# Kernel optimization log

Hardware: AMD Instinct MI355X
Metric: run time of the kernel (lower is better)

Reference implementation:

```python
import jax, jax.numpy as jnp
import numpy as np
from jax import lax
from functools import lru_cache

WS = 8       # window size
SS = 4       # shift size
NH = 8       # attention heads
D_STATE = 64
D_CONV = 4
CHUNK = 256  # SSD chunk length


def _ln(x, w, b, eps=1e-5):
    mu = x.mean(-1, keepdims=True)
    xc = x - mu
    var = (xc * xc).mean(-1, keepdims=True)
    return xc * lax.rsqrt(var + eps) * w + b


@lru_cache(maxsize=None)
def _rel_index(ws):
    coords = np.stack(np.meshgrid(np.arange(ws), np.arange(ws), indexing='ij')).reshape(2, -1)
    rel = (coords[:, :, None] - coords[:, None, :]).transpose(1, 2, 0)
    rel[:, :, 0] += ws - 1
    rel[:, :, 1] += ws - 1
    rel[:, :, 0] *= 2 * ws - 1
    return jnp.asarray(rel.sum(-1))  # (N, N)


@lru_cache(maxsize=None)
def _shift_mask(H, W, ws, ss):
    img = np.zeros((H, W))
    cnt = 0
    for hs in (slice(0, -ws), slice(-ws, -ss), slice(-ss, None)):
        for wsl in (slice(0, -ws), slice(-ws, -ss), slice(-ss, None)):
            img[hs, wsl] = cnt
            cnt += 1
    mw = img.reshape(H // ws, ws, W // ws, ws).transpose(0, 2, 1, 3).reshape(-1, ws * ws)
    diff = mw[:, None, :] - mw[:, :, None]
    return jnp.asarray(np.where(diff != 0, -100.0, 0.0).astype(np.float32))  # (nW,N,N)


def _segsum(a):
    # a: (...,Q) -> (...,Q,Q) with S[i,j] = sum_{k=j+1..i} a_k for i>=j else -inf
    T = a.shape[-1]
    cs = jnp.cumsum(a, -1)
    d = cs[..., :, None] - cs[..., None, :]
    return jnp.where(jnp.tril(jnp.ones((T, T), bool)), d, -jnp.inf)


def _ssd(xd, a, Bc, Cc):
    # Chunked SSD scan (Mamba2). xd=(B,L,H,P) pre-multiplied by dt; a=dt*A (B,L,H);
    # Bc,Cc=(B,L,N) with ngroups=1 (shared across heads).
    B_, L, H_, P = xd.shape
    Q = CHUNK
    c = L // Q
    N = Bc.shape[-1]
    xd = xd.reshape(B_, c, Q, H_, P)
    a = a.reshape(B_, c, Q, H_).transpose(0, 3, 1, 2)  # (B,H,c,Q)
    Bc = Bc.reshape(B_, c, Q, N)
    Cc = Cc.reshape(B_, c, Q, N)
    A_cs = jnp.cumsum(a, -1)
    Lm = jnp.exp(_segsum(a))  # (B,H,c,Q,Q) causal decay mask
    Yd = jnp.einsum('bcln,bcsn,bhcls,bcshp->bclhp', Cc, Bc, Lm, xd)
    dec_st = jnp.exp(A_cs[..., -1:] - A_cs)
    states = jnp.einsum('bcsn,bhcs,bcshp->bchpn', Bc, dec_st, xd)  # (B,c,H,P,N)
    chunk_dec = jnp.exp(A_cs[..., -1])  # (B,H,c)

    def step(h, inp):
        dec, st = inp
        return h * dec[..., None, None] + st, h

    h0 = jnp.zeros((B_, H_, P, N), xd.dtype)
    _, st_in = lax.scan(step, h0, (chunk_dec.transpose(2, 0, 1), states.transpose(1, 0, 2, 3, 4)))
    st_in = st_in.transpose(1, 0, 2, 3, 4)  # (B,c,H,P,N) state entering each chunk
    Yo = jnp.einsum('bcln,bchpn,bhcl->bclhp', Cc, st_in, jnp.exp(A_cs))
    return (Yd + Yo).reshape(B_, L, H_, P)


def _mamba2(x, win, conv_w, conv_b, dt_bias, a_log, d_skip, norm_w, wout):
    Bb, L, _ = x.shape
    conv_dim = conv_w.shape[0]
    d_inner = conv_dim - 2 * D_STATE
    nh = a_log.shape[0]
    hd = d_inner // nh
    zxbcdt = x @ win
    z = zxbcdt[..., :d_inner]
    xBC = zxbcdt[..., d_inner:d_inner + conv_dim]
    dt = zxbcdt[..., -nh:]
    # causal depthwise conv (kernel D_CONV) + SiLU
    xp = jnp.pad(xBC, ((0, 0), (D_CONV - 1, 0), (0, 0)))
    xc = conv_b + sum(xp[:, k:k + L, :] * conv_w[:, k] for k in range(D_CONV))
    xc = jax.nn.silu(xc)
    xs = xc[..., :d_inner].reshape(Bb, L, nh, hd)
    Bm = xc[..., d_inner:d_inner + D_STATE]
    Cm = xc[..., d_inner + D_STATE:]
    dt = jax.nn.softplus(dt + dt_bias)  # (B,L,nh)
    a = dt * (-jnp.exp(a_log))
    y = _ssd(xs * dt[..., None], a, Bm, Cm)
    y = y + d_skip[None, None, :, None] * xs
    y = y.reshape(Bb, L, d_inner)
    u = y * jax.nn.silu(z)  # gated RMSNorm
    u = u * lax.rsqrt((u * u).mean(-1, keepdims=True) + 1e-5) * norm_w
    return u @ wout


def reference(x, ln1_w, ln1_b, ns_w, ns_b, m_win, m_conv_w, m_conv_b, m_dt_bias,
              m_a_log, m_d, m_norm_w, m_wout, tm_w1, tm_b1, tm_w2, tm_b2, nt_w, nt_b,
              qkv_w, qkv_b, rpb, gate_w, gate_b, proj_w, proj_b,
              cg_w1a, cg_b1a, cg_w2a, cg_b2a, cg_w1m, cg_b1m, cg_w2m, cg_b2m, cg_wf, cg_bf,
              ln2_w, ln2_b, mlp_w1, mlp_b1, mlp_w2, mlp_b2, H, W):
    twoB, L, C = x.shape
    B = twoB // 2
    shortcut = x
    xn = _ln(x, ln1_w, ln1_b)
    # ---- Branch A: factorized SSM (spatial Mamba2 + symmetric temporal MLP fusion) ----
    xns = _ln(xn, ns_w, ns_b)
    sp = _mamba2(xns, m_win, m_conv_w, m_conv_b, m_dt_bias, m_a_log, m_d, m_norm_w, m_wout) + xn
    f0, f1 = sp[:B], sp[B:]

    def tmix(a, b):
        h = jax.nn.silu(jnp.concatenate([a, b], -1) @ tm_w1 + tm_b1)
        return h @ tm_w2 + tm_b2

    f0 = _ln(f0 + tmix(f0, f1), nt_w, nt_b)
    f1 = _ln(f1 + tmix(f1, f0), nt_w, nt_b)
    xm = jnp.concatenate([f0, f1], 0)
    # ---- Branch B: shifted-window gated attention ----
    N = WS * WS
    x2 = jnp.roll(xn.reshape(twoB, H, W, C), (-SS, -SS), (1, 2))
    xw = x2.reshape(twoB, H // WS, WS, W // WS, WS, C).transpose(0, 1, 3, 2, 4, 5).reshape(-1, N, C)
    qkv = (xw @ qkv_w + qkv_b).reshape(-1, N, 3, NH, C // NH).transpose(2, 0, 3, 1, 4)
    q, k, v = qkv[0], qkv[1], qkv[2]  # (nWB, NH, N, hd)
    attn = (q * (C // NH) ** -0.5) @ k.transpose(0, 1, 3, 2)
    attn = attn + rpb[_rel_index(WS)].transpose(2, 0, 1)[None]
    mask = _shift_mask(H, W, WS, SS)
    nW = mask.shape[0]
    attn = (attn.reshape(twoB, nW, NH, N, N) + mask[None, :, None]).reshape(-1, NH, N, N)
    attn = jax.nn.softmax(attn, -1)
    out = (attn @ v).transpose(0, 2, 1, 3).reshape(-1, N, C)
    out = out * jax.nn.sigmoid(xw @ gate_w + gate_b)  # per-token gate
    out = out @ proj_w + proj_b
    out = out.reshape(twoB, H // WS, W // WS, WS, WS, C).transpose(0, 1, 3, 2, 4, 5).reshape(twoB, H, W, C)
    xa = jnp.roll(out, (SS, SS), (1, 2)).reshape(twoB, L, C)
    # ---- Cross-gating fusion (1x1-conv bottleneck gates == per-position MLPs) ----
    gm = jax.nn.sigmoid(jax.nn.relu(xa @ cg_w1a + cg_b1a) @ cg_w2a + cg_b2a)
    ga = jax.nn.sigmoid(jax.nn.relu(xm @ cg_w1m + cg_b1m) @ cg_w2m + cg_b2m)
    fused = jnp.concatenate([xm * gm, xa * ga], -1) @ cg_wf + cg_bf
    xo = shortcut + fused
    # ---- MLP ----
    h = jax.nn.gelu(_ln(xo, ln2_w, ln2_b) @ mlp_w1 + mlp_b1, approximate=False)
    return xo + h @ mlp_w2 + mlp_b2


def setup_inputs():
    key = jax.random.key(0)
    ks = iter(jax.random.split(key, 64))

    def nrm(shape, s=0.02):
        return jax.random.normal(next(ks), shape, jnp.float32) * s

    C, d_inner, nh_m = 256, 512, 8
    twoB, H, W = 8, 64, 64
    L = H * W
    conv_dim = d_inner + 2 * D_STATE
    inp = dict(
        x=jax.random.normal(next(ks), (twoB, L, C), jnp.float32),
        ln1_w=jnp.ones(C), ln1_b=jnp.zeros(C),
        ns_w=jnp.ones(C), ns_b=jnp.zeros(C),
        m_win=nrm((C, 2 * d_inner + 2 * D_STATE + nh_m)),
        m_conv_w=nrm((conv_dim, D_CONV), 0.1), m_conv_b=jnp.zeros(conv_dim),
        m_dt_bias=nrm((nh_m,), 0.1),
        m_a_log=jnp.log(jnp.arange(1, nh_m + 1, dtype=jnp.float32)),
        m_d=jnp.ones(nh_m), m_norm_w=jnp.ones(d_inner), m_wout=nrm((d_inner, C)),
        tm_w1=nrm((2 * C, C)), tm_b1=jnp.zeros(C), tm_w2=nrm((C, C)), tm_b2=jnp.zeros(C),
        nt_w=jnp.ones(C), nt_b=jnp.zeros(C),
        qkv_w=nrm((C, 3 * C)), qkv_b=jnp.zeros(3 * C),
        rpb=nrm(((2 * WS - 1) ** 2, NH)),
        gate_w=nrm((C, C)), gate_b=jnp.zeros(C),
        proj_w=nrm((C, C)), proj_b=jnp.zeros(C),
        cg_w1a=nrm((C, C // 4)), cg_b1a=jnp.zeros(C // 4), cg_w2a=nrm((C // 4, C)), cg_b2a=jnp.zeros(C),
        cg_w1m=nrm((C, C // 4)), cg_b1m=jnp.zeros(C // 4), cg_w2m=nrm((C // 4, C)), cg_b2m=jnp.zeros(C),
        cg_wf=nrm((2 * C, C)), cg_bf=jnp.zeros(C),
        ln2_w=jnp.ones(C), ln2_b=jnp.zeros(C),
        mlp_w1=nrm((C, 4 * C)), mlp_b1=jnp.zeros(4 * C),
        mlp_w2=nrm((4 * C, C)), mlp_b2=jnp.zeros(C),
        H=H, W=W,
    )
    return inp
```

## Files before the change

kernel.cpp:

```cpp
#include <hip/hip_runtime.h>
#include <math.h>


#define DEVI static __device__ __forceinline__
typedef unsigned short u16;
typedef unsigned int   u32;
typedef __attribute__((ext_vector_type(8))) short s16x8;
typedef __attribute__((ext_vector_type(4))) float f32x4;

DEVI float sigm_(float x){ return 1.f/(1.f+__expf(-x)); }
DEVI float silu_(float x){ return x/(1.f+__expf(-x)); }
DEVI float wsum_(float v){
#pragma unroll
  for (int o=32;o>0;o>>=1) v += __shfl_xor(v,o,64);
  return v;
}

DEVI float b2f(u16 u){ union{u32 i; float f;} v; v.i = ((u32)u)<<16; return v.f; }
DEVI u16 f2b(float f){ union{float f; u32 i;} v; v.f=f; u32 r = v.i + 0x7fffu + ((v.i>>16)&1u); return (u16)(r>>16); }
DEVI float4 ld4(const float* p){ return *(const float4*)p; }
DEVI float4 ld4(const u16* p){
  uint2 r = *(const uint2*)p;
  return make_float4(b2f((u16)(r.x&0xffff)), b2f((u16)(r.x>>16)),
                     b2f((u16)(r.y&0xffff)), b2f((u16)(r.y>>16)));
// ... 229 lines not shown
    if (gk < K1) av = ld4(A1 + (size_t)(m0+arow)*K1 + gk);
    else         av = ld4(A2 + (size_t)(m0+arow)*K2 + (gk-K1));
    as[ac4+0][arow]=av.x; as[ac4+1][arow]=av.y; as[ac4+2][arow]=av.z; as[ac4+3][arow]=av.w;
    int gn = n0 + bnc;
    const float* wp = W + (size_t)(k0+bkr)*ldw;
    if (gn+3 < N) {
      *(float4*)&bs[bkr][bnc] = *(const float4*)(wp + gn);
    } else {
#pragma unroll
      for (int j=0;j<4;j++) bs[bkr][bnc+j] = (gn+j<N) ? wp[gn+j] : 0.f;
    }
    __syncthreads();
#pragma unroll
    for (int kk=0; kk<16; kk++){
      float4 a4 = *(const float4*)&as[kk][ty*4];
      float4 b4 = *(const float4*)&bs[kk][tx*4];
      acc[0][0]+=a4.x*b4.x; acc[0][1]+=a4.x*b4.y; acc[0][2]+=a4.x*b4.z; acc[0][3]+=a4.x*b4.w;
      acc[1][0]+=a4.y*b4.x; acc[1][1]+=a4.y*b4.y; acc[1][2]+=a4.y*b4.z; acc[1][3]+=a4.y*b4.w;
      acc[2][0]+=a4.z*b4.x; acc[2][1]+=a4.z*b4.y; acc[2][2]+=a4.z*b4.z; acc[2][3]+=a4.z*b4.w;
      acc[3][0]+=a4.w*b4.x; acc[3][1]+=a4.w*b4.y; acc[3][2]+=a4.w*b4.z; acc[3][3]+=a4.w*b4.w;
    }
    __syncthreads();
  }
#pragma unroll
  for (int i=0;i<4;i++){
    int gm = m0 + ty*4 + i;
#pragma unroll
    for (int j=0;j<4;j++){
      int gn = n0 + tx*4 + j;
      if (gn >= N) continue;
      float v = acc[i][j] + (bias ? bias[gn] : 0.f);
      size_t off = (size_t)gm*N + gn;
      if (EPI==EPI_SILU)        v = silu_(v);
      else if (EPI==EPI_GELU)   v = 0.5f*v*(1.f+erff(v*0.70710678118654752f));
      else if (EPI==EPI_SIGMUL) v = tof(other[off])*sigm_(v);
      else if (EPI==EPI_ADD)    v = v + tof(other[off]);
      else if (EPI==EPI_RELU)   v = fmaxf(v,0.f);
      else if (EPI==EPI_SIGMOID)v = sigm_(v);
      sto(outp + off, v);
    }
  }
}

__global__ __launch_bounds__(256) void xbcconv_k(
    const u16* __restrict__ A1, const u16* __restrict__ Wt,
    const float* __restrict__ cw, const float* __restrict__ cb,
    u16* __restrict__ XC, u16* __restrict__ XT)
{
  __shared__ u16 As[64][40];
  __shared__ u16 Ab[16][40];
  __shared__ u16 Bs[128][40];
  __shared__ float Cls[67][132];
  int m0 = blockIdx.y*64, n0 = blockIdx.x*128;
  bool first = ((m0 & 4095) == 0);
  int t = threadIdx.x;
  int lane = t&63, w = t>>6;
  int wr = w>>1, wc = w&1;
  int lg = lane>>4, li = lane&15;
  f32x4 acc[2][4], acc3[2];
#pragma unroll
  for (int mi=0;mi<2;mi++)
#pragma unroll
    for (int ni=0;ni<4;ni++) acc[mi][ni] = (f32x4){0.f,0.f,0.f,0.f};
  acc3[0]=(f32x4){0,0,0,0}; acc3[1]=(f32x4){0,0,0,0};
  for (int i=t; i<320; i+=256) ((u32*)&Ab[0][0])[i] = 0u;
  int lrow = t>>2, lc8 = (t&3)*8;
  for (int k0=0; k0<256; k0+=32){
    *(uint4*)&As[lrow][lc8] = *(const uint4*)(A1 + (size_t)(m0+lrow)*256 + k0 + lc8);
    if (t < 12 && !first){
      int r3 = t>>2, seg = t&3;
      *(uint4*)&Ab[r3][seg*8] = *(const uint4*)(A1 + (size_t)(m0-3+r3)*256 + k0 + seg*8);
    }
#pragma unroll
    for (int i=0;i<2;i++){
      int row = lrow + i*64;
      *(uint4*)&Bs[row][lc8] = *(const uint4*)(Wt + (size_t)(n0+row)*256 + k0 + lc8);
    }
    __syncthreads();
    s16x8 afr[2], bfr[4];
#pragma unroll
    for (int mi=0;mi<2;mi++)
      afr[mi] = *(const s16x8*)&As[wr*32+mi*16+li][lg*8];
#pragma unroll
    for (int ni=0;ni<4;ni++)
      bfr[ni] = *(const s16x8*)&Bs[wc*64+ni*16+li][lg*8];
#pragma unroll
    for (int mi=0;mi<2;mi++)
#pragma unroll
      for (int ni=0;ni<4;ni++)
        acc[mi][ni] = __builtin_amdgcn_mfma_f32_16x16x32_bf16(afr[mi], bfr[ni], acc[mi][ni], 0,0,0);
    {
      s16x8 abf = *(const s16x8*)&Ab[li][lg*8];
#pragma unroll
      for (int ni2=0;ni2<2;ni2++){
        s16x8 bb = *(const s16x8*)&Bs[w*32+ni2*16+li][lg*8];
        acc3[ni2] = __builtin_amdgcn_mfma_f32_16x16x32_bf16(abf, bb, acc3[ni2], 0,0,0);
      }
    }
    __syncthreads();
  }
#pragma unroll
  for (int mi=0;mi<2;mi++)
#pragma unroll
    for (int ni=0;ni<4;ni++){
      int col = wc*64 + ni*16 + li;
#pragma unroll
      for (int r=0;r<4;r++){
        int rl = wr*32 + mi*16 + lg*4 + r;
        Cls[3+rl][col] = acc[mi][ni][r];
      }
    }
  if (lg == 0){
#pragma unroll
    for (int ni2=0;ni2<2;ni2++){
      int col = w*32 + ni2*16 + li;
#pragma unroll
      for (int r=0;r<3;r++)
        Cls[r][col] = acc3[ni2][r];
    }
  }
  __syncthreads();
  int col = t & 127, half = t >> 7;
  int ch = n0 + col;
  float w0 = cw[ch*4+0], w1 = cw[ch*4+1], w2 = cw[ch*4+2], w3 = cw[ch*4+3];
  float bias = cb[ch];
  int r0 = half*32;
  float c0 = Cls[r0+0][col], c1 = Cls[r0+1][col], c2 = Cls[r0+2][col];
  u16 xtbuf[32];
  if (ch < 512){
#pragma unroll
    for (int rr=0; rr<32; rr++){
      float c3 = Cls[r0+rr+3][col];
      float v = bias + w0*c0 + w1*c1 + w2*c2 + w3*c3;
      xtbuf[rr] = f2b(silu_(v));
      c0=c1; c1=c2; c2=c3;
    }
    int g = m0 >> 8;
    u16* dst = XT + ((size_t)(g*512 + ch))*256 + (m0&255) + r0;
#pragma unroll
    for (int q=0;q<4;q++) *(uint4*)(dst + q*8) = *(const uint4*)&xtbuf[q*8];
  } else {
#pragma unroll
    for (int rr=0; rr<32; rr++){
      float c3 = Cls[r0+rr+3][col];
      float v = bias + w0*c0 + w1*c1 + w2*c2 + w3*c3;
      XC[(size_t)(m0 + r0 + rr)*128 + (ch-512)] = f2b(silu_(v));
      c0=c1; c1=c2; c2=c3;
    }
  }
}

__global__ __launch_bounds__(256) void acs_k(
    const float* __restrict__ DTRAW, const float* __restrict__ dtb, const float* __restrict__ alog,
    float* __restrict__ DT_, float* __restrict__ ACS_)
{
  int wid = (blockIdx.x<<2) + (threadIdx.x>>6);
  int lane = threadIdx.x & 63;
  int c  = wid & 15;
  int bh = wid >> 4;
  int b  = bh >> 3, h = bh & 7;
  float db = dtb[h];
  float ea = __expf(alog[h]);
  size_t tok0 = (size_t)b*4096 + c*256 + lane*4;
  float v0,v1,v2,v3;
  {
    float xv, sp;
    xv = DTRAW[(tok0+0)*8 + h] + db; sp = (xv>20.f)?xv:log1pf(__expf(xv)); DT_[(tok0+0)*8+h]=sp; v0 = -sp*ea;
    xv = DTRAW[(tok0+1)*8 + h] + db; sp = (xv>20.f)?xv:log1pf(__expf(xv)); DT_[(tok0+1)*8+h]=sp; v1 = -sp*ea;
    xv = DTRAW[(tok0+2)*8 + h] + db; sp = (xv>20.f)?xv:log1pf(__expf(xv)); DT_[(tok0+2)*8+h]=sp; v2 = -sp*ea;
    xv = DTRAW[(tok0+3)*8 + h] + db; sp = (xv>20.f)?xv:log1pf(__expf(xv)); DT_[(tok0+3)*8+h]=sp; v3 = -sp*ea;
  }
  v1 += v0; v2 += v1; v3 += v2;
  float tot = v3, s = tot;
#pragma unroll
  for (int o=1;o<64;o<<=1){
    float u = __shfl_up(s, o, 64);
    if (lane >= o) s += u;
  }
  float excl = s - tot;
  float* dst = ACS_ + (size_t)bh*4096 + c*256 + lane*4;
  dst[0]=excl+v0; dst[1]=excl+v1; dst[2]=excl+v2; dst[3]=excl+v3;
}

__global__ __launch_bounds__(256) void states_k(
    const u16* __restrict__ XC, const u16* __restrict__ XT,
    const float* __restrict__ DTc, const float* __restrict__ ACSc,
    float* __restrict__ ST)
{
  int b = blockIdx.x;
  int j = b & 7, s = b >> 3;
  int h = s & 7, gq = s >> 3;
  int g = j + gq*8;
  int c = g & 15, bl = g >> 4;
  __shared__ u16 Xt[64*64];
  __shared__ u16 Bt[64*64];
  int t = threadIdx.x;
  int lane = t&63, w = t>>6;
  int wr = w>>1, wc = w&1;
  int lg = lane>>4, li = lane&15;
  const float* acs = ACSc + ((size_t)(bl*8+h))*4096 + c*256;
  float aL = acs[255];
  size_t tok0 = (size_t)bl*4096 + c*256;
  f32x4 acc[2][2];
#pragma unroll
  for (int mi=0;mi<2;mi++)
#pragma unroll
    for (int ni=0;ni<2;ni++) acc[mi][ni] = (f32x4){0.f,0.f,0.f,0.f};
  int sr = t>>2, cg = t&3;
  int srch = sr>>3, srlo = sr&7;
  const u16* xtb = XT + ((size_t)(g*512) + h*64)*256;
  for (int s0=0; s0<256; s0+=64){
    __syncthreads();
    {
      int prow = t>>2, c2 = t&3;
      const u16* src = xtb + (size_t)prow*256 + s0;
      uint4 a0 = *(const uint4*)(src + c2*8);
      uint4 a1 = *(const uint4*)(src + (c2+4)*8);
      *(uint4*)&Xt[prow*64 + (vswz(prow,c2)<<3)]   = a0;
      *(uint4*)&Xt[prow*64 + (vswz(prow,c2+4)<<3)] = a1;
    }
    {
      size_t grow = tok0 + s0 + sr;
      float scl = __expf(aL - acs[s0+sr]) * DTc[grow*8 + h];
      const u16* brow_p = XC + grow*128 + cg*16;
      uint4 ba = *(const uint4*)brow_p, bb2 = *(const uint4*)(brow_p+8);
      const u16* bu = (const u16*)&ba;
#pragma unroll
      for (int jj=0;jj<8;jj++){
        int row = cg*16+jj;
        Bt[row*64 + (vswz(row,srch)<<3) + srlo] = f2b(b2f(bu[jj])*scl);
      }
      const u16* bu2 = (const u16*)&bb2;
#pragma unroll
      for (int jj=0;jj<8;jj++){
        int row = cg*16+8+jj;
        Bt[row*64 + (vswz(row,srch)<<3) + srlo] = f2b(b2f(bu2[jj])*scl);
      }
    }
    __syncthreads();
    s16x8 afr[2][2], bfr[2][2];
#pragma unroll
    for (int kk=0;kk<2;kk++){
#pragma unroll
      for (int mi=0;mi<2;mi++){
        int row = wr*32+mi*16+li;
        afr[mi][kk] = *(const s16x8*)&Xt[row*64 + (vswz(row, kk*4+lg)<<3)];
      }
#pragma unroll
      for (int ni=0;ni<2;ni++){
        int row = wc*32+ni*16+li;
        bfr[ni][kk] = *(const s16x8*)&Bt[row*64 + (vswz(row, kk*4+lg)<<3)];
      }
    }
#pragma unroll
    for (int kk=0;kk<2;kk++)
#pragma unroll
      for (int mi=0;mi<2;mi++)
#pragma unroll
        for (int ni=0;ni<2;ni++)
          acc[mi][ni] = __builtin_amdgcn_mfma_f32_16x16x32_bf16(afr[mi][kk], bfr[ni][kk], acc[mi][ni], 0,0,0);
  }
  float* dst = ST + ((size_t)(g*8 + h))*4096;
#pragma unroll
  for (int mi=0;mi<2;mi++)
#pragma unroll
    for (int ni=0;ni<2;ni++){
      int gn = wc*32 + ni*16 + li;
#pragma unroll
      for (int r=0;r<4;r++){
        int gp = wr*32 + mi*16 + lg*4 + r;
        dst[gp*64 + gn] = acc[mi][ni][r];
      }
    }
}

__global__ __launch_bounds__(256) void scan_k(
    const float* __restrict__ ST, const float* __restrict__ ACSc, u16* __restrict__ STIN)
{
  int bid = blockIdx.x;
  int eq = bid & 3, h = (bid>>2)&7, bl = bid>>5;
  int t = threadIdx.x;
  float hr[4] = {0.f,0.f,0.f,0.f};
  for (int c=0;c<16;c++){
    float dec = __expf(ACSc[((size_t)(bl*8+h))*4096 + c*256 + 255]);
    size_t base = ((size_t)((bl*16+c)*8+h))*4096 + (size_t)eq*1024;
#pragma unroll
    for (int e=0;e<4;e++){
      size_t idx = base + e*256 + t;
      float st = ST[idx];
      STIN[idx] = f2b(hr[e]);
      hr[e] = hr[e]*dec + st;
    }
  }
}

__global__ __launch_bounds__(256) void ydy_k(
    const u16* __restrict__ XC, const u16* __restrict__ XT,
    const float* __restrict__ DTc,
    const float* __restrict__ ACSc, const u16* __restrict__ STIN,
    const float* __restrict__ dskip, u16* __restrict__ Y)
{
  int b = blockIdx.x;
  int j = b & 7, s = b >> 3;
  int ltp = s & 1, h = (s>>1) & 7, gq = s >> 4;
  int g = j + gq*8;
  int c = g & 15, bl = g >> 4;
  __shared__ u16 Ct[64][72];
  __shared__ u16 Sb[64][72];
  __shared__ u16 Sl[64][72];
  __shared__ u16 Vt[64*64];
  int t = threadIdx.x;
  int lane = t&63, w = t>>6;
  int wr = w>>1, wc = w&1;
  int lg = lane>>4, li = lane&15;
  const float* acs = ACSc + ((size_t)(bl*8+h))*4096 + c*256;
  size_t tok0 = (size_t)bl*4096 + c*256;
  int sr = t>>2;
  int cg = t&3;
  const u16* stin = STIN + ((size_t)(g*8+h))*4096;
  const u16* xtb = XT + ((size_t)(g*512) + h*64)*256;
  float dsk = dskip[h];
  for (int pp=0; pp<2; pp++){
    int lt = pp ? (3-ltp) : ltp;
    int l0 = lt*64;
#pragma unroll
    for (int it=0; it<2; it++){
      int seg = (t&3) + it*4;
      *(uint4*)&Ct[sr][seg*8] = *(const uint4*)(XC + (tok0+l0+sr)*128 + 64 + seg*8);
    }
    float acsl[2][4];
#pragma unroll
    for (int mi=0;mi<2;mi++)
#pragma unroll
      for (int r=0;r<4;r++)
        acsl[mi][r] = acs[l0 + wr*32 + mi*16 + lg*4 + r];
    f32x4 accP[2][2], accO[2][2];
#pragma unroll
    for (int mi=0;mi<2;mi++)
#pragma unroll
      for (int ni=0;ni<2;ni++){ accP[mi][ni]=(f32x4){0,0,0,0}; accO[mi][ni]=(f32x4){0,0,0,0}; }
    __syncthreads();
#pragma unroll
    for (int kk=0;kk<2;kk++){
      s16x8 bfr[2];
#pragma unroll
      for (int ni=0;ni<2;ni++){
        int p = wc*32 + ni*16 + li;
        bfr[ni] = *(const s16x8*)(stin + p*64 + kk*32 + lg*8);
      }
#pragma unroll
      for (int mi=0;mi<2;mi++){
        s16x8 afr = *(const s16x8*)&Ct[wr*32+mi*16+li][kk*32+lg*8];
#pragma unroll
        for (int ni=0;ni<2;ni++)
          accO[mi][ni] = __builtin_amdgcn_mfma_f32_16x16x32_bf16(afr, bfr[ni], accO[mi][ni], 0,0,0);
      }
    }
    for (int sb=0; sb<=lt; sb++){
      int s0 = sb*64;
      __syncthreads();
#pragma unroll
      for (int it=0; it<2; it++){
        int seg = (t&3) + it*4;
        *(uint4*)&Sb[sr][seg*8] = *(const uint4*)(XC + (tok0+s0+sr)*128 + seg*8);
      }
      {
        int prow = t>>2, c2 = t&3;
        const u16* src = xtb + (size_t)prow*256 + s0;
        uint4 a0 = *(const uint4*)(src + c2*8);
        uint4 a1 = *(const uint4*)(src + (c2+4)*8);
        *(uint4*)&Vt[prow*64 + (vswz(prow,c2)<<3)]   = a0;
        *(uint4*)&Vt[prow*64 + (vswz(prow,c2+4)<<3)] = a1;
      }
      __syncthreads();
      f32x4 sacc[2][2];
#pragma unroll
      for (int mi=0;mi<2;mi++)
#pragma unroll
        for (int ni=0;ni<2;ni++) sacc[mi][ni]=(f32x4){0,0,0,0};
#pragma unroll
      for (int kk=0;kk<2;kk++){
        s16x8 bfr[2];
#pragma unroll
        for (int ni=0;ni<2;ni++)
          bfr[ni] = *(const s16x8*)&Sb[wc*32+ni*16+li][kk*32+lg*8];
#pragma unroll
        for (int mi=0;mi<2;mi++){
          s16x8 afr = *(const s16x8*)&Ct[wr*32+mi*16+li][kk*32+lg*8];
#pragma unroll
          for (int ni=0;ni<2;ni++)
            sacc[mi][ni] = __builtin_amdgcn_mfma_f32_16x16x32_bf16(afr, bfr[ni], sacc[mi][ni], 0,0,0);
        }
      }
#pragma unroll
      for (int ni=0;ni<2;ni++){
        int cs2 = wc*32 + ni*16 + li;
        int gsj = s0 + cs2;
        float acss = acs[gsj];
        float dts = DTc[(tok0+gsj)*8 + h];
#pragma unroll
        for (int mi=0;mi<2;mi++){
#pragma unroll
          for (int r=0;r<4;r++){
            int lrow = wr*32 + mi*16 + lg*4 + r;
            int gl = l0 + lrow;
            float wgt = (gsj <= gl) ? __expf(acsl[mi][r] - acss)*dts : 0.f;
            Sl[lrow][cs2] = f2b(sacc[mi][ni][r] * wgt);
          }
        }
      }
      __syncthreads();
#pragma unroll
      for (int kk=0;kk<2;kk++){
        s16x8 bfr[2];
#pragma unroll
        for (int ni=0;ni<2;ni++){
          int p = wc*32+ni*16+li;
          bfr[ni] = *(const s16x8*)&Vt[p*64 + (vswz(p, kk*4+lg)<<3)];
        }
#pragma unroll
        for (int mi=0;mi<2;mi++){
          s16x8 afr = *(const s16x8*)&Sl[wr*32+mi*16+li][kk*32+lg*8];
#pragma unroll
          for (int ni=0;ni<2;ni++)
            accP[mi][ni] = __builtin_amdgcn_mfma_f32_16x16x32_bf16(afr, bfr[ni], accP[mi][ni], 0,0,0);
        }
      }
    }
    __syncthreads();
#pragma unroll
    for (int mi=0;mi<2;mi++){
#pragma unroll
      for (int ni=0;ni<2;ni++){
        int p = wc*32 + ni*16 + li;
#pragma unroll
        for (int r=0;r<4;r++){
          int lrow = wr*32 + mi*16 + lg*4 + r;
          float el = __expf(acsl[mi][r]);
          float xsv = b2f(Vt[p*64 + (vswz(p, lrow>>3)<<3) + (lrow&7)]);
          Sb[lrow][p] = f2b(accP[mi][ni][r] + el*accO[mi][ni][r] + dsk*xsv);
        }
      }
    }
    __syncthreads();
#pragma unroll
    for (int it=0; it<2; it++){
      int seg = (t&3) + it*4;
      *(uint4*)(Y + (tok0+l0+sr)*512 + h*64 + seg*8) = *(const uint4*)&Sb[sr][seg*8];
    }
  }
}

__global__ __launch_bounds__(256) void urms_k(
    u16* Y, const u16* __restrict__ Z, const float* __restrict__ nw)
{
  int tok = blockIdx.x*4 + (threadIdx.x>>6);
  int lane = threadIdx.x & 63;
  size_t base = (size_t)tok*512 + lane*8;
  float y[8], z[8], u[8];
  ld8(Y+base, y); ld8(Z+base, z);
  float ss=0.f;
#pragma unroll
  for (int e=0;e<8;e++){ u[e] = y[e]*silu_(z[e]); ss += u[e]*u[e]; }
  ss = wsum_(ss);
  float r = rsqrtf(ss*(1.f/512.f) + 1e-5f);
  float4 w0 = *(const float4*)(nw + lane*8);
  float4 w1 = *(const float4*)(nw + lane*8 + 4);
  float o[8];
  o[0]=u[0]*r*w0.x; o[1]=u[1]*r*w0.y; o[2]=u[2]*r*w0.z; o[3]=u[3]*r*w0.w;
  o[4]=u[4]*r*w1.x; o[5]=u[5]*r*w1.y; o[6]=u[6]*r*w1.z; o[7]=u[7]*r*w1.w;
  st8(Y+base, o);
}

__global__ __launch_bounds__(256) void attn_k(
    const u16* __restrict__ QKV, const float* __restrict__ rpb, u16* __restrict__ OW)
{
  int win = blockIdx.x;
  int wid = win & 63;
  int head = blockIdx.y;
  __shared__ u16 Qs[64][40];
  __shared__ u16 Ks[64][40];
  __shared__ u16 Vt[32][72];
  __shared__ u16 Pl[64][72];
  __shared__ float rl[225];
  __shared__ int rid[64];
  int t = threadIdx.x;
  int lane = t&63, w = t>>6;
  int lg = lane>>4, li = lane&15;
  const float scale = 0.17677669529663687f;
  {
    int row = t>>2, seg = t&3;
    const u16* base = QKV + ((size_t)win*64 + row)*768 + head*32 + seg*8;
    uint4 q = *(const uint4*)base;
    const u16* qe = (const u16*)&q;
    u16 qs8[8];
#pragma unroll
    for (int jq=0;jq<8;jq++) qs8[jq] = f2b(b2f(qe[jq])*scale);
    *(uint4*)&Qs[row][seg*8] = *(const uint4*)qs8;
    *(uint4*)&Ks[row][seg*8] = *(const uint4*)(base + 256);
    uint4 v = *(const uint4*)(base + 512);
    const u16* ve = (const u16*)&v;
#pragma unroll
    for (int jq=0;jq<8;jq++) Vt[seg*8+jq][row] = ve[jq];
  }
  if (t < 225) rl[t] = rpb[t*8 + head];
  if (t < 64){
    int h2 = ((wid>>3)<<3) + (t>>3);
    int w2 = ((wid&7)<<3) + (t&7);
    int rh = (h2<56)?0:((h2<60)?1:2);
    int rw = (w2<56)?0:((w2<60)?1:2);
    rid[t] = rh*3 + rw;
  }
  __syncthreads();
  f32x4 sc[4];
  {
    s16x8 qf = *(const s16x8*)&Qs[w*16+li][lg*8];
#pragma unroll
    for (int ni=0;ni<4;ni++){
      s16x8 kf = *(const s16x8*)&Ks[ni*16+li][lg*8];
      sc[ni] = __builtin_amdgcn_mfma_f32_16x16x32_bf16(qf, kf, (f32x4){0,0,0,0}, 0,0,0);
    }
  }
  float inv[4];
#pragma unroll
  for (int r=0;r<4;r++){
    int i = w*16 + lg*4 + r;
    int ridi = rid[i];
    float vv[4];
    float m = -1e30f;
#pragma unroll
    for (int ni=0;ni<4;ni++){
      int jj = ni*16 + li;
      float sv = sc[ni][r] + rl[((i>>3)-(jj>>3)+7)*15 + ((i&7)-(jj&7)+7)];
      if (ridi != rid[jj]) sv -= 100.f;
      vv[ni] = sv;
      m = fmaxf(m, sv);
    }
#pragma unroll
    for (int o=1;o<16;o<<=1) m = fmaxf(m, __shfl_xor(m, o, 64));
    float sum = 0.f;
#pragma unroll
    for (int ni=0;ni<4;ni++){ vv[ni] = __expf(vv[ni]-m); sum += vv[ni]; }
#pragma unroll
    for (int o=1;o<16;o<<=1) sum += __shfl_xor(sum, o, 64);
    inv[r] = 1.f/sum;
#pragma unroll
    for (int ni=0;ni<4;ni++) Pl[i][ni*16+li] = f2b(vv[ni]);
  }
  __syncthreads();
  f32x4 oacc[2];
  oacc[0]=(f32x4){0,0,0,0}; oacc[1]=(f32x4){0,0,0,0};
#pragma unroll
  for (int kk=0;kk<2;kk++){
    s16x8 pf = *(const s16x8*)&Pl[w*16+li][kk*32+lg*8];
#pragma unroll
    for (int ni=0;ni<2;ni++){
      s16x8 vf = *(const s16x8*)&Vt[ni*16+li][kk*32+lg*8];
      oacc[ni] = __builtin_amdgcn_mfma_f32_16x16x32_bf16(pf, vf, oacc[ni], 0,0,0);
    }
  }
#pragma unroll
  for (int ni=0;ni<2;ni++)
#pragma unroll
    for (int r=0;r<4;r++)
      Pl[w*16+lg*4+r][ni*16+li] = f2b(oacc[ni][r]*inv[r]);
  __syncthreads();
  {
    int row = t>>2, seg = t&3;
    *(uint4*)(OW + ((size_t)win*64 + row)*256 + head*32 + seg*8) = *(const uint4*)&Pl[row][seg*8];
  }
}

extern "C" void kernel_launch(void* const* d_in, const int* in_sizes, int n_in,
                              void* d_out, int out_size, void* d_ws, size_t ws_size,
                              hipStream_t stream)
{
  (void)in_sizes; (void)n_in; (void)out_size;
  const size_t OFF_XN   = 0;
  const size_t OFF_XNS  = 16777216;
  const size_t OFF_SP   = 33554432;
  const size_t OFF_DTRAW= 50331648;
  const size_t OFF_DT   = 51380224;
  const size_t OFF_ACS  = 53477376;
  const size_t OFF_WTS  = 54525952;
  const size_t ARO      = 58195968;
  int NB = 0;
  if      (ws_size >= ARO + 8ull*14680064) NB = 8;
  else if (ws_size >= ARO + 4ull*14680064) NB = 4;
  else if (ws_size >= ARO + 2ull*14680064) NB = 2;
  else if (ws_size >= ARO + 1ull*14680064) NB = 1;
  else return;
  int NC = 8 / NB;
  int RJ = (NB==8)?32768 : (NB==4)?16384 : (NB==2)?8192 : 4096;

  const float* x       = (const float*)d_in[0];
  const float* ln1_w   = (const float*)d_in[1];
  const float* ln1_b   = (const float*)d_in[2];
  const float* ns_w    = (const float*)d_in[3];
  const float* ns_b    = (const float*)d_in[4];
  const float* m_win   = (const float*)d_in[5];
  const float* m_conv_w= (const float*)d_in[6];
  const float* m_conv_b= (const float*)d_in[7];
  const float* m_dt_b  = (const float*)d_in[8];
  const float* m_a_log = (const float*)d_in[9];
  const float* m_d     = (const float*)d_in[10];
  const float* m_norm_w= (const float*)d_in[11];
  const float* m_wout  = (const float*)d_in[12];
  const float* tm_w1   = (const float*)d_in[13];
  const float* tm_b1   = (const float*)d_in[14];
  const float* tm_w2   = (const float*)d_in[15];
  const float* tm_b2   = (const float*)d_in[16];
  const float* nt_w    = (const float*)d_in[17];
  const float* nt_b    = (const float*)d_in[18];
  const float* qkv_w   = (const float*)d_in[19];
  const float* qkv_b   = (const float*)d_in[20];
  const float* rpb     = (const float*)d_in[21];
  const float* gate_w  = (const float*)d_in[22];
  const float* gate_b  = (const float*)d_in[23];
  const float* proj_w  = (const float*)d_in[24];
  const float* proj_b  = (const float*)d_in[25];
  const float* cg_w1a  = (const float*)d_in[26];
  const float* cg_b1a  = (const float*)d_in[27];
  const float* cg_w2a  = (const float*)d_in[28];
  const float* cg_b2a  = (const float*)d_in[29];
  const float* cg_w1m  = (const float*)d_in[30];
  const float* cg_b1m  = (const float*)d_in[31];
  const float* cg_w2m  = (const float*)d_in[32];
  const float* cg_b2m  = (const float*)d_in[33];
  const float* cg_wf   = (const float*)d_in[34];
  const float* cg_bf   = (const float*)d_in[35];
  const float* ln2_w   = (const float*)d_in[36];
  const float* ln2_b   = (const float*)d_in[37];
  const float* mlp_w1  = (const float*)d_in[38];
  const float* mlp_b1  = (const float*)d_in[39];
  const float* mlp_w2  = (const float*)d_in[40];
  const float* mlp_b2  = (const float*)d_in[41];
  float* dout = (float*)d_out;
  char* ws = (char*)d_ws;

  u16*  XN   = (u16*)(ws + OFF_XN);
  u16*  XNS  = (u16*)(ws + OFF_XNS);
  u16*  SP   = (u16*)(ws + OFF_SP);
  float* DTRAW = (float*)(ws + OFF_DTRAW);
  float* DT  = (float*)(ws + OFF_DT);
  float* ACS = (float*)(ws + OFF_ACS);
  u16*  WTS  = (u16*)(ws + OFF_WTS);
  u16* WT_XBC = WTS + 0;
  u16* WT_Z   = WTS + 163840;
  u16* WT_WOUT= WTS + 294912;
  u16* WT_TM1 = WTS + 425984;
  u16* WT_TM2 = WTS + 491520;
  u16* WT_QKV = WTS + 557056;
  u16* WT_GATE= WTS + 753664;
  u16* WT_PROJ= WTS + 819200;
  u16* WT_W2A = WTS + 884736;
  u16* WT_W2M = WTS + 901120;
  u16* WT_WF  = WTS + 917504;
  u16* WT_MLP1= WTS + 1048576;
  u16* WT_MLP2= WTS + 1310720;
  u16* WT_W1A = WTS + 1572864;
  u16* WT_W1M = WTS + 1589248;
  char* AR = ws + ARO;
  u16*  XCc   = (u16*)AR;
  u16*  Zc    = (u16*)(AR + (size_t)NB*5242880);
  u16*  XTc   = Zc;
  u16*  STINc = (u16*)(AR + (size_t)NB*9437184);
  float* STc  = (float*)(AR + (size_t)NB*10485760);
  u16*  Yc    = (u16*)(AR + (size_t)NB*10485760);
  u16*  QKVc  = (u16*)AR;
  u16*  OWc   = (u16*)(AR + (size_t)NB*6291456);
  u16*  TBUF  = (u16*)AR;
  u16*  XM    = XNS;
  u16*  XA    = XN;
  u16*  CGHA  = (u16*)AR;
  u16*  CGHM  = (u16*)(AR + 4194304);
  u16*  LNc   = (u16*)AR;
  u16*  MHc   = (u16*)(AR + (size_t)RJ*512);

  const size_t TB = 4096*256;
  const size_t H2 = 16384*256;

  WtTab tab;
  tab.d[0]  = { m_win+512, WT_XBC, 1160, 256, 8, 20 };
  tab.d[1]  = { m_win,     WT_Z,   1160, 256, 8, 16 };
  tab.d[2]  = { m_wout,    WT_WOUT, 256, 512, 16, 8 };
  tab.d[3]  = { tm_w1,     WT_TM1,  256, 512, 16, 8 };
  tab.d[4]  = { tm_w2,     WT_TM2,  256, 256, 8, 8 };
  tab.d[5]  = { qkv_w,     WT_QKV,  768, 256, 8, 24 };
  tab.d[6]  = { gate_w,    WT_GATE, 256, 256, 8, 8 };
  tab.d[7]  = { proj_w,    WT_PROJ, 256, 256, 8, 8 };
  tab.d[8]  = { cg_w2a,    WT_W2A,  256, 64, 2, 8 };
  tab.d[9]  = { cg_w2m,    WT_W2M,  256, 64, 2, 8 };
  tab.d[10] = { cg_wf,     WT_WF,   256, 512, 16, 8 };
  tab.d[11] = { mlp_w1,    WT_MLP1,1024, 256, 8, 32 };
  tab.d[12] = { mlp_w2,    WT_MLP2, 256,1024, 32, 8 };
  tab.d[13] = { cg_w1a,    WT_W1A,   64, 256, 8, 2 };
  tab.d[14] = { cg_w1m,    WT_W1M,   64, 256, 8, 2 };
  int ntiles = 0;
  for (int i=0;i<15;i++) ntiles += tab.d[i].kb * tab.d[i].nt;
  wtall_k<<<ntiles,256,0,stream>>>(tab);

  ln2x_k<<<8192,256,0,stream>>>(x, ln1_w, ln1_b, ns_w, ns_b, XN, XNS);
  gemm_k<EPI_NONE,float,float><<<dim3(1,512),256,0,stream>>>(XNS,nullptr,256,0, m_win+1152,1160, nullptr, nullptr, DTRAW, 32768,8);
  acs_k<<<256,256,0,stream>>>(DTRAW, m_dt_b, m_a_log, DT, ACS);

  for (int cc=0; cc<NC; cc++){
    int cb0 = cc*NB;
    const u16* XNSc = XNS + (size_t)cb0*TB;
    const float* DTcp = DT + (size_t)cb0*32768;
    const float* ACScp = ACS + (size_t)cb0*32768;
    xbcconv_k<<<dim3(5,NB*64),256,0,stream>>>(XNSc, WT_XBC, m_conv_w, m_conv_b, XCc, XTc);
    states_k<<<NB*128,256,0,stream>>>(XCc, XTc, DTcp, ACScp, STc);
    scan_k<<<NB*32,256,0,stream>>>(STc, ACScp, STINc);
    ydy_k<<<NB*256,256,0,stream>>>(XCc, XTc, DTcp, ACScp, STINc, m_d, Yc);
    mgemm_k<128,128,EPI_NONE,false,false,float,u16><<<dim3(4,NB*32),256,0,stream>>>(XNSc,nullptr,256,0, WT_Z, nullptr, nullptr, Zc, 512, 0);
    urms_k<<<NB*1024,256,0,stream>>>(Yc, Zc, m_norm_w);
    mgemm_k<64,128,EPI_ADD,false,false,u16,u16><<<dim3(2,NB*64),256,0,stream>>>(Yc,nullptr,512,0, WT_WOUT, nullptr, XN + (size_t)cb0*TB, SP + (size_t)cb0*TB, 256, 0);
  }

  mgemm_k<64,128,EPI_SILU,false,false,float,u16><<<dim3(2,256),256,0,stream>>>(SP, SP+H2, 256,256, WT_TM1, tm_b1, nullptr, TBUF, 256, 0);
  mgemm_k<64,128,EPI_ADD,false,false,u16,u16><<<dim3(2,256),256,0,stream>>>(TBUF,nullptr,256,0, WT_TM2, tm_b2, SP, XM, 256, 0);
  ln_k<u16><<<4096,256,0,stream>>>(XM, nt_w, nt_b, XM);
  mgemm_k<64,128,EPI_SILU,false,false,float,u16><<<dim3(2,256),256,0,stream>>>(SP+H2, XM, 256,256, WT_TM1, tm_b1, nullptr, TBUF, 256, 0);
  mgemm_k<64,128,EPI_ADD,false,false,u16,u16><<<dim3(2,256),256,0,stream>>>(TBUF,nullptr,256,0, WT_TM2, tm_b2, SP+H2, XM+H2, 256, 0);
  ln_k<u16><<<4096,256,0,stream>>>(XM+H2, nt_w, nt_b, XM+H2);

  for (int cc=0; cc<NC; cc++){
    int r0 = cc*NB*4096;
    mgemm_k<128,128,EPI_NONE,true,false,float,u16><<<dim3(6,NB*32),256,0,stream>>>(XN,nullptr,256,0, WT_QKV, qkv_b, nullptr, QKVc, 768, r0);
    attn_k<<<dim3(NB*64,8),256,0,stream>>>(QKVc, rpb, OWc);
    mgemm_k<64,128,EPI_SIGMUL,true,false,u16,u16><<<dim3(2,NB*64),256,0,stream>>>(XN,nullptr,256,0, WT_GATE, gate_b, OWc, OWc, 256, r0);
    mgemm_k<64,128,EPI_NONE,false,true,float,u16><<<dim3(2,NB*64),256,0,stream>>>(OWc,nullptr,256,0, WT_PROJ, proj_b, nullptr, XA, 256, r0);
  }

  mgemm_k<128,64,EPI_RELU,false,false,float,u16><<<dim3(1,256),256,0,stream>>>(XA,nullptr,256,0, WT_W1A, cg_b1a, nullptr, CGHA, 64, 0);
  mgemm_k<128,64,EPI_RELU,false,false,float,u16><<<dim3(1,256),256,0,stream>>>(XM,nullptr,256,0, WT_W1M, cg_b1m, nullptr, CGHM, 64, 0);
  mgemm_k<64,128,EPI_SIGMUL,false,false,u16,u16><<<dim3(2,512),256,0,stream>>>(CGHA,nullptr,64,0, WT_W2A, cg_b2a, XM, XM, 256, 0);
  mgemm_k<64,128,EPI_SIGMUL,false,false,u16,u16><<<dim3(2,512),256,0,stream>>>(CGHM,nullptr,64,0, WT_W2M, cg_b2m, XA, XA, 256, 0);
  mgemm_k<64,128,EPI_ADD,false,false,float,float><<<dim3(2,512),256,0,stream>>>(XM, XA, 256,256, WT_WF, cg_bf, x, dout, 256, 0);

  for (int q=0; q<32768/RJ; q++){
    float* XOq = dout + (size_t)q*RJ*256;
    ln_k<float><<<RJ/4,256,0,stream>>>(XOq, ln2_w, ln2_b, LNc);
    mgemm_k<128,128,EPI_GELU,false,false,float,u16><<<dim3(8,RJ/128),256,0,stream>>>(LNc,nullptr,256,0, WT_MLP1, mlp_b1, nullptr, MHc, 1024, 0);
    mgemm_k<64,128,EPI_ADD,false,false,float,float><<<dim3(2,RJ/64),256,0,stream>>>(MHc,nullptr,1024,0, WT_MLP2, mlp_b2, XOq, XOq, 256, 0);
  }
}
```

Measured before the change: 566.3 us.

## Process two heads per ydy block to reuse C·Bᵀ scores and C tile

The ydy kernel now handles a pair of heads per block, so the C tile and the per-subblock C·Bᵀ score MFMA are computed once and reused for both heads. Only the decay-weighting and the value GEMM are done per head. The inter-chunk state contribution is folded into the accumulator up front, and the grid is halved. This trades extra LDS (a second V tile), more registers and extra barriers per iteration for less duplicated score computation and fewer C loads.

Result: faster. 547.0 us (-3.4%).

```diff
diff --git a/kernel.cpp b/kernel.cpp
--- a/kernel.cpp
+++ b/kernel.cpp
@@ -555,24 +555,28 @@
 {
   int b = blockIdx.x;
   int j = b & 7, s = b >> 3;
-  int ltp = s & 1, h = (s>>1) & 7, gq = s >> 4;
+  int hp = s & 3, ltp = (s>>2) & 1, gq = s >> 3;
   int g = j + gq*8;
   int c = g & 15, bl = g >> 4;
+  int h0 = hp*2, h1 = h0 + 1;
   __shared__ u16 Ct[64][72];
   __shared__ u16 Sb[64][72];
   __shared__ u16 Sl[64][72];
-  __shared__ u16 Vt[64*64];
+  __shared__ u16 Vt0[64*64];
+  __shared__ u16 Vt1[64*64];
   int t = threadIdx.x;
   int lane = t&63, w = t>>6;
   int wr = w>>1, wc = w&1;
   int lg = lane>>4, li = lane&15;
-  const float* acs = ACSc + ((size_t)(bl*8+h))*4096 + c*256;
+  const float* acs0 = ACSc + ((size_t)(bl*8+h0))*4096 + c*256;
+  const float* acs1 = ACSc + ((size_t)(bl*8+h1))*4096 + c*256;
   size_t tok0 = (size_t)bl*4096 + c*256;
   int sr = t>>2;
-  int cg = t&3;
-  const u16* stin = STIN + ((size_t)(g*8+h))*4096;
-  const u16* xtb = XT + ((size_t)(g*512) + h*64)*256;
-  float dsk = dskip[h];
+  const u16* stin0 = STIN + ((size_t)(g*8+h0))*4096;
+  const u16* stin1 = STIN + ((size_t)(g*8+h1))*4096;
+  const u16* xtb0 = XT + ((size_t)(g*512) + h0*64)*256;
+  const u16* xtb1 = XT + ((size_t)(g*512) + h1*64)*256;
+  float dsk0 = dskip[h0], dsk1 = dskip[h1];
   for (int pp=0; pp<2; pp++){
     int lt = pp ? (3-ltp) : ltp;
     int l0 = lt*64;
@@ -581,37 +585,79 @@
       int seg = (t&3) + it*4;
       *(uint4*)&Ct[sr][seg*8] = *(const uint4*)(XC + (tok0+l0+sr)*128 + 64 + seg*8);
     }
-    float acsl[2][4];
+    float acsl0[2][4], acsl1[2][4];
 #pragma unroll
     for (int mi=0;mi<2;mi++)
 #pragma unroll
-      for (int r=0;r<4;r++)
-        acsl[mi][r] = acs[l0 + wr*32 + mi*16 + lg*4 + r];
-    f32x4 accP[2][2], accO[2][2];
-#pragma unroll
-    for (int mi=0;mi<2;mi++)
-#pragma unroll
-      for (int ni=0;ni<2;ni++){ accP[mi][ni]=(f32x4){0,0,0,0}; accO[mi][ni]=(f32x4){0,0,0,0}; }
+      for (int r=0;r<4;r++){
+        int idx = l0 + wr*32 + mi*16 + lg*4 + r;
+        acsl0[mi][r] = acs0[idx];
+        acsl1[mi][r] = acs1[idx];
+      }
+    f32x4 accP0[2][2], accP1[2][2];
     __syncthreads();
-#pragma unroll
-    for (int kk=0;kk<2;kk++){
-      s16x8 bfr[2];
-#pragma unroll
-      for (int ni=0;ni<2;ni++){
-        int p = wc*32 + ni*16 + li;
-        bfr[ni] = *(const s16x8*)(stin + p*64 + kk*32 + lg*8);
-      }
-#pragma unroll
-      for (int mi=0;mi<2;mi++){
-        s16x8 afr = *(const s16x8*)&Ct[wr*32+mi*16+li][kk*32+lg*8];
+    {
+      f32x4 aO[2][2];
+#pragma unroll
+      for (int mi=0;mi<2;mi++)
+#pragma unroll
+        for (int ni=0;ni<2;ni++) aO[mi][ni]=(f32x4){0,0,0,0};
+#pragma unroll
+      for (int kk=0;kk<2;kk++){
+        s16x8 bfr[2];
+#pragma unroll
+        for (int ni=0;ni<2;ni++){
+          int p = wc*32 + ni*16 + li;
+          bfr[ni] = *(const s16x8*)(stin0 + p*64 + kk*32 + lg*8);
+        }
+#pragma unroll
+        for (int mi=0;mi<2;mi++){
+          s16x8 afr = *(const s16x8*)&Ct[wr*32+mi*16+li][kk*32+lg*8];
+#pragma unroll
+          for (int ni=0;ni<2;ni++)
+            aO[mi][ni] = __builtin_amdgcn_mfma_f32_16x16x32_bf16(afr, bfr[ni], aO[mi][ni], 0,0,0);
+        }
+      }
+#pragma unroll
+      for (int mi=0;mi<2;mi++)
 #pragma unroll
         for (int ni=0;ni<2;ni++)
-          accO[mi][ni] = __builtin_amdgcn_mfma_f32_16x16x32_bf16(afr, bfr[ni], accO[mi][ni], 0,0,0);
-      }
+#pragma unroll
+          for (int r=0;r<4;r++)
+            accP0[mi][ni][r] = __expf(acsl0[mi][r]) * aO[mi][ni][r];
+    }
+    {
+      f32x4 aO[2][2];
+#pragma unroll
+      for (int mi=0;mi<2;mi++)
+#pragma unroll
+        for (int ni=0;ni<2;ni++) aO[mi][ni]=(f32x4){0,0,0,0};
+#pragma unroll
+      for (int kk=0;kk<2;kk++){
+        s16x8 bfr[2];
+#pragma unroll
+        for (int ni=0;ni<2;ni++){
+          int p = wc*32 + ni*16 + li;
+          bfr[ni] = *(const s16x8*)(stin1 + p*64 + kk*32 + lg*8);
+        }
+#pragma unroll
+        for (int mi=0;mi<2;mi++){
+          s16x8 afr = *(const s16x8*)&Ct[wr*32+mi*16+li][kk*32+lg*8];
+#pragma unroll
+          for (int ni=0;ni<2;ni++)
+            aO[mi][ni] = __builtin_amdgcn_mfma_f32_16x16x32_bf16(afr, bfr[ni], aO[mi][ni], 0,0,0);
+        }
+      }
+#pragma unroll
+      for (int mi=0;mi<2;mi++)
+#pragma unroll
+        for (int ni=0;ni<2;ni++)
+#pragma unroll
+          for (int r=0;r<4;r++)
+            accP1[mi][ni][r] = __expf(acsl1[mi][r]) * aO[mi][ni][r];
     }
     for (int sb=0; sb<=lt; sb++){
       int s0 = sb*64;
-      __syncthreads();
 #pragma unroll
       for (int it=0; it<2; it++){
         int seg = (t&3) + it*4;
@@ -619,11 +665,16 @@
       }
       {
         int prow = t>>2, c2 = t&3;
-        const u16* src = xtb + (size_t)prow*256 + s0;
-        uint4 a0 = *(const uint4*)(src + c2*8);
-        uint4 a1 = *(const uint4*)(src + (c2+4)*8);
-        *(uint4*)&Vt[prow*64 + (vswz(prow,c2)<<3)]   = a0;
-        *(uint4*)&Vt[prow*64 + (vswz(prow,c2+4)<<3)] = a1;
+        const u16* src0 = xtb0 + (size_t)prow*256 + s0;
+        uint4 a0 = *(const uint4*)(src0 + c2*8);
+        uint4 a1 = *(const uint4*)(src0 + (c2+4)*8);
+        *(uint4*)&Vt0[prow*64 + (vswz(prow,c2)<<3)]   = a0;
+        *(uint4*)&Vt0[prow*64 + (vswz(prow,c2+4)<<3)] = a1;
+        const u16* src1 = xtb1 + (size_t)prow*256 + s0;
+        uint4 b0 = *(const uint4*)(src1 + c2*8);
+        uint4 b1 = *(const uint4*)(src1 + (c2+4)*8);
+        *(uint4*)&Vt1[prow*64 + (vswz(prow,c2)<<3)]   = b0;
+        *(uint4*)&Vt1[prow*64 + (vswz(prow,c2+4)<<3)] = b1;
       }
       __syncthreads();
       f32x4 sacc[2][2];
@@ -649,15 +700,15 @@
       for (int ni=0;ni<2;ni++){
         int cs2 = wc*32 + ni*16 + li;
         int gsj = s0 + cs2;
-        float acss = acs[gsj];
-        float dts = DTc[(tok0+gsj)*8 + h];
+        float acss = acs0[gsj];
+        float dts = DTc[(tok0+gsj)*8 + h0];
 #pragma unroll
         for (int mi=0;mi<2;mi++){
 #pragma unroll
           for (int r=0;r<4;r++){
             int lrow = wr*32 + mi*16 + lg*4 + r;
             int gl = l0 + lrow;
-            float wgt = (gsj <= gl) ? __expf(acsl[mi][r] - acss)*dts : 0.f;
+            float wgt = (gsj <= gl) ? __expf(acsl0[mi][r] - acss)*dts : 0.f;
             Sl[lrow][cs2] = f2b(sacc[mi][ni][r] * wgt);
           }
         }
@@ -669,18 +720,53 @@
 #pragma unroll
         for (int ni=0;ni<2;ni++){
           int p = wc*32+ni*16+li;
-          bfr[ni] = *(const s16x8*)&Vt[p*64 + (vswz(p, kk*4+lg)<<3)];
+          bfr[ni] = *(const s16x8*)&Vt0[p*64 + (vswz(p, kk*4+lg)<<3)];
         }
 #pragma unroll
         for (int mi=0;mi<2;mi++){
           s16x8 afr = *(const s16x8*)&Sl[wr*32+mi*16+li][kk*32+lg*8];
 #pragma unroll
           for (int ni=0;ni<2;ni++)
-            accP[mi][ni] = __builtin_amdgcn_mfma_f32_16x16x32_bf16(afr, bfr[ni], accP[mi][ni], 0,0,0);
-        }
-      }
-    }
-    __syncthreads();
+            accP0[mi][ni] = __builtin_amdgcn_mfma_f32_16x16x32_bf16(afr, bfr[ni], accP0[mi][ni], 0,0,0);
+        }
+      }
+      __syncthreads();
+#pragma unroll
+      for (int ni=0;ni<2;ni++){
+        int cs2 = wc*32 + ni*16 + li;
+        int gsj = s0 + cs2;
+        float acss = acs1[gsj];
+        float dts = DTc[(tok0+gsj)*8 + h1];
+#pragma unroll
+        for (int mi=0;mi<2;mi++){
+#pragma unroll
+          for (int r=0;r<4;r++){
+            int lrow = wr*32 + mi*16 + lg*4 + r;
+            int gl = l0 + lrow;
+            float wgt = (gsj <= gl) ? __expf(acsl1[mi][r] - acss)*dts : 0.f;
+            Sl[lrow][cs2] = f2b(sacc[mi][ni][r] * wgt);
+          }
+        }
+      }
+      __syncthreads();
+#pragma unroll
+      for (int kk=0;kk<2;kk++){
+        s16x8 bfr[2];
+#pragma unroll
+        for (int ni=0;ni<2;ni++){
+          int p = wc*32+ni*16+li;
+          bfr[ni] = *(const s16x8*)&Vt1[p*64 + (vswz(p, kk*4+lg)<<3)];
+        }
+#pragma unroll
+        for (int mi=0;mi<2;mi++){
+          s16x8 afr = *(const s16x8*)&Sl[wr*32+mi*16+li][kk*32+lg*8];
+#pragma unroll
+          for (int ni=0;ni<2;ni++)
+            accP1[mi][ni] = __builtin_amdgcn_mfma_f32_16x16x32_bf16(afr, bfr[ni], accP1[mi][ni], 0,0,0);
+        }
+      }
+      __syncthreads();
+    }
 #pragma unroll
     for (int mi=0;mi<2;mi++){
 #pragma unroll
@@ -689,9 +775,11 @@
 #pragma unroll
         for (int r=0;r<4;r++){
           int lrow = wr*32 + mi*16 + lg*4 + r;
-          float el = __expf(acsl[mi][r]);
-          float xsv = b2f(Vt[p*64 + (vswz(p, lrow>>3)<<3) + (lrow&7)]);
-          Sb[lrow][p] = f2b(accP[mi][ni][r] + el*accO[mi][ni][r] + dsk*xsv);
+          int voff = p*64 + (vswz(p, lrow>>3)<<3) + (lrow&7);
+          float xsv0 = b2f(Vt0[voff]);
+          float xsv1 = b2f(Vt1[voff]);
+          Sb[lrow][p] = f2b(accP0[mi][ni][r] + dsk0*xsv0);
+          Ct[lrow][p] = f2b(accP1[mi][ni][r] + dsk1*xsv1);
         }
       }
     }
@@ -699,8 +787,10 @@
 #pragma unroll
     for (int it=0; it<2; it++){
       int seg = (t&3) + it*4;
-      *(uint4*)(Y + (tok0+l0+sr)*512 + h*64 + seg*8) = *(const uint4*)&Sb[sr][seg*8];
-    }
+      *(uint4*)(Y + (tok0+l0+sr)*512 + h0*64 + seg*8) = *(const uint4*)&Sb[sr][seg*8];
+      *(uint4*)(Y + (tok0+l0+sr)*512 + h1*64 + seg*8) = *(const uint4*)&Ct[sr][seg*8];
+    }
+    __syncthreads();
   }
 }
 
@@ -965,7 +1055,7 @@
     xbcconv_k<<<dim3(5,NB*64),256,0,stream>>>(XNSc, WT_XBC, m_conv_w, m_conv_b, XCc, XTc);
     states_k<<<NB*128,256,0,stream>>>(XCc, XTc, DTcp, ACScp, STc);
     scan_k<<<NB*32,256,0,stream>>>(STc, ACScp, STINc);
-    ydy_k<<<NB*256,256,0,stream>>>(XCc, XTc, DTcp, ACScp, STINc, m_d, Yc);
+    ydy_k<<<NB*128,256,0,stream>>>(XCc, XTc, DTcp, ACScp, STINc, m_d, Yc);
     mgemm_k<128,128,EPI_NONE,false,false,float,u16><<<dim3(4,NB*32),256,0,stream>>>(XNSc,nullptr,256,0, WT_Z, nullptr, nullptr, Zc, 512, 0);
     urms_k<<<NB*1024,256,0,stream>>>(Yc, Zc, m_norm_w);
     mgemm_k<64,128,EPI_ADD,false,false,u16,u16><<<dim3(2,NB*64),256,0,stream>>>(Yc,nullptr,512,0, WT_WOUT, nullptr, XN + (size_t)cb0*TB, SP + (size_t)cb0*TB, 256, 0);
```
